# Performance work log

Measured on AMD Instinct MI355X. Metric: run time of the kernel, lower is better.

Reference implementation:

```python
import jax, jax.numpy as jnp
import numpy as np

D_MODEL = 1024   # 'seq_len' arg = input feature dim
FF_DIM = 1024
SCALE = 0.03125  # 1/sqrt(1024)


def setup_inputs() -> dict:
    key = jax.random.key(0)
    ks = jax.random.split(key, 7)
    B, T = 8, 2048
    s = 1.0 / np.sqrt(D_MODEL)
    return {
        "sequence": jax.random.normal(ks[0], (B, T, D_MODEL), dtype=jnp.float32),
        "Wq": jax.random.uniform(ks[1], (FF_DIM, D_MODEL), jnp.float32, -s, s),
        "bq": jax.random.uniform(ks[2], (FF_DIM,), jnp.float32, -s, s),
        "Wk": jax.random.uniform(ks[3], (FF_DIM, D_MODEL), jnp.float32, -s, s),
        "bk": jax.random.uniform(ks[4], (FF_DIM,), jnp.float32, -s, s),
        "Wv": jax.random.uniform(ks[5], (FF_DIM, D_MODEL), jnp.float32, -s, s),
        "bv": jax.random.uniform(ks[6], (FF_DIM,), jnp.float32, -s, s),
    }


def reference(sequence, Wq, bq, Wk, bk, Wv, bv):
    # Q/K/V linear projections (torch Linear: x @ W.T + b)
    q = jnp.einsum('btd,fd->btf', sequence, Wq) + bq
    k = jnp.einsum('btd,fd->btf', sequence, Wk) + bk
    v = jnp.einsum('btd,fd->btf', sequence, Wv) + bv
    # scaled dot-product attention (dropout p=0 -> identity)
    scores = jnp.einsum('btf,bsf->bts', q, k) * SCALE  # [B,T,T]
    attn = jax.nn.softmax(scores, axis=-1)
    return jnp.einsum('bts,bsf->btf', attn, v)
```

## Files before the change

### kernel.cpp

```cpp
#include <hip/hip_runtime.h>
#include <hip/hip_bf16.h>

#define BB 8
#define TT 2048
#define DD 1024
#define FF 1024

typedef __attribute__((ext_vector_type(8))) short bf16x8;
typedef __attribute__((ext_vector_type(4))) float f32x4;
typedef __attribute__((ext_vector_type(4))) short s16x4;

constexpr float kScaleLog2e = 0.03125f * 1.44269504088896340736f;

__device__ __forceinline__ short bf16_bits(float x) {
    __hip_bfloat16 h = __float2bfloat16(x);
    short s;
    __builtin_memcpy(&s, &h, sizeof(short));
    return s;
}

__global__ __launch_bounds__(256) void cvt_all(
    const float* __restrict__ seq, const float* __restrict__ Wq,
    const float* __restrict__ Wk, const float* __restrict__ Wv,
    short* __restrict__ seqb, short* __restrict__ Wb)
{
    const int bid = blockIdx.x;
    const float* src;
    short* dst;
    int i;
    if (bid < 8192)      { src = seq; dst = seqb;                      i = bid * 256 + threadIdx.x; }
    else if (bid < 8704) { src = Wq;  dst = Wb;                        i = (bid - 8192) * 256 + threadIdx.x; }
    else if (bid < 9216) { src = Wk;  dst = Wb + (size_t)FF * DD;      i = (bid - 8704) * 256 + threadIdx.x; }
    else                 { src = Wv;  dst = Wb + (size_t)2 * FF * DD;  i = (bid - 9216) * 256 + threadIdx.x; }
    f32x4 a = ((const f32x4*)src)[2 * i];
    f32x4 b = ((const f32x4*)src)[2 * i + 1];
    bf16x8 o;
#pragma unroll
    for (int j = 0; j < 4; ++j) { o[j] = bf16_bits(a[j]); o[4 + j] = bf16_bits(b[j]); }
    ((bf16x8*)dst)[i] = o;
}

__device__ __forceinline__ void gemm_core(
    const short* __restrict__ A, int lda, int m0,
    const short* __restrict__ B, int ldb, int n0,
    int K, short* As, short* Bs, f32x4 acc[4][4])
{
    const int tid  = threadIdx.x;
    const int lane = tid & 63;
    const int w    = tid >> 6;
    const int wm   = (w & 1) * 64;
    const int wn   = (w >> 1) * 64;
    const int r    = lane & 15;
    const int qd   = lane >> 4;

    for (int k0 = 0; k0 < K; k0 += 64) {
        __syncthreads();
#pragma unroll
        for (int it = 0; it < 4; ++it) {
            const int s   = tid + it * 256;
            const int row = s >> 3;
            const int col = (((s & 7) - (row & 7)) & 7) << 3;
            __builtin_amdgcn_global_load_lds(
                (const __attribute__((address_space(1))) unsigned int*)
                    (A + (size_t)(m0 + row) * lda + k0 + col),
                (__attribute__((address_space(3))) unsigned int*)(As + s * 8),
                16, 0, 0);
            __builtin_amdgcn_global_load_lds(
                (const __attribute__((address_space(1))) unsigned int*)
                    (B + (size_t)(n0 + row) * ldb + k0 + col),
                (__attribute__((address_space(3))) unsigned int*)(Bs + s * 8),
                16, 0, 0);
        }
        __syncthreads();
#pragma unroll
        for (int kk = 0; kk < 2; ++kk) {
            bf16x8 af[4], bf[4];
#pragma unroll
            for (int m = 0; m < 4; ++m) {
                const int R = wm + m * 16 + r;
                af[m] = *(const bf16x8*)(As + R * 64 + (((kk * 4 + qd) + R) & 7) * 8);
            }
#pragma unroll
            for (int n = 0; n < 4; ++n) {
                const int R = wn + n * 16 + r;
                bf[n] = *(const bf16x8*)(Bs + R * 64 + (((kk * 4 + qd) + R) & 7) * 8);
            }
#pragma unroll
            for (int m = 0; m < 4; ++m)
#pragma unroll
                for (int n = 0; n < 4; ++n)
                    acc[m][n] = __builtin_amdgcn_mfma_f32_16x16x32_bf16(af[m], bf[n], acc[m][n], 0, 0, 0);
        }
    }
}

__global__ __launch_bounds__(256) void qkv_tiled(
    const short* __restrict__ seqb, const short* __restrict__ Wb,
    const float* __restrict__ bq, const float* __restrict__ bk,
    const float* __restrict__ bv,
    __hip_bfloat16* __restrict__ q, __hip_bfloat16* __restrict__ k,
    __hip_bfloat16* __restrict__ vT)
{
    __shared__ short As[128 * 64], Bs[128 * 64];
    const int bid  = blockIdx.x;
    const int mt   = bid / 24;
    const int rest = bid % 24;
    const int nt   = rest & 7;
    const int proj = rest >> 3;

    const short* W    = Wb + (size_t)proj * FF * DD;
    const float* bias = proj == 0 ? bq : (proj == 1 ? bk : bv);

    f32x4 acc[4][4];
#pragma unroll
    for (int m = 0; m < 4; ++m)
#pragma unroll
        for (int n = 0; n < 4; ++n) acc[m][n] = (f32x4){0.f, 0.f, 0.f, 0.f};

    gemm_core(seqb, DD, mt * 128, W, DD, nt * 128, DD, As, Bs, acc);

    const int lane = threadIdx.x & 63;
    const int w    = threadIdx.x >> 6;
    const int wm   = (w & 1) * 64;
    const int wn   = (w >> 1) * 64;
    const int r    = lane & 15;
    const int qd   = lane >> 4;
    const int row_base = mt * 128 + wm + qd * 4;
    const int col_base = nt * 128 + wn + r;

    if (proj < 2) {
        __hip_bfloat16* dst = (proj == 0) ? q : k;
#pragma unroll
        for (int n = 0; n < 4; ++n) {
            const int col = col_base + n * 16;
            const float bv_ = bias[col];
#pragma unroll
            for (int m = 0; m < 4; ++m)
#pragma unroll
                for (int i = 0; i < 4; ++i)
                    dst[(size_t)(row_base + m * 16 + i) * FF + col] =
                        __float2bfloat16(acc[m][n][i] + bv_);
        }
    } else {
#pragma unroll
        for (int m = 0; m < 4; ++m) {
            const int rowg = row_base + m * 16;
            const int b_   = rowg >> 11;
            const int t_   = rowg & 2047;
            __hip_bfloat16* vb = vT + (size_t)b_ * FF * TT;
#pragma unroll
            for (int n = 0; n < 4; ++n) {
                const int col = col_base + n * 16;
                const float bv_ = bias[col];
                s16x4 pack;
#pragma unroll
                for (int i = 0; i < 4; ++i) pack[i] = bf16_bits(acc[m][n][i] + bv_);
                *(s16x4*)(vb + (size_t)col * TT + t_) = pack;
            }
        }
    }
}

__global__ __launch_bounds__(256) void score_tiled(
    const __hip_bfloat16* __restrict__ q, const __hip_bfloat16* __restrict__ k,
    __hip_bfloat16* __restrict__ P, float* __restrict__ Z)
{
    __shared__ short As[128 * 64], Bs[128 * 64];
    const int bid = blockIdx.x;
    const int b   = bid >> 8;
    const int rem = bid & 255;
    const int tt  = rem >> 4;
    const int st  = rem & 15;

    const short* qb = (const short*)q + (size_t)b * TT * FF;
    const short* kb = (const short*)k + (size_t)b * TT * FF;

    f32x4 acc[4][4];
#pragma unroll
    for (int m = 0; m < 4; ++m)
#pragma unroll
        for (int n = 0; n < 4; ++n) acc[m][n] = (f32x4){0.f, 0.f, 0.f, 0.f};

    gemm_core(qb, FF, tt * 128, kb, FF, st * 128, FF, As, Bs, acc);

    const int lane = threadIdx.x & 63;
    const int w    = threadIdx.x >> 6;
    const int wm   = (w & 1) * 64;
    const int wn   = (w >> 1) * 64;
    const int r    = lane & 15;
    const int qd   = lane >> 4;
    const int row_base = tt * 128 + wm + qd * 4;
    const int col_base = st * 128 + wn + r;

    __hip_bfloat16* Pb = P + (size_t)b * TT * TT;
    float* Zb = Z + b * TT;

    float rs[4][4];
#pragma unroll
    for (int m = 0; m < 4; ++m)
#pragma unroll
        for (int i = 0; i < 4; ++i) rs[m][i] = 0.f;

#pragma unroll
    for (int m = 0; m < 4; ++m)
#pragma unroll
        for (int n = 0; n < 4; ++n) {
            const int col = col_base + n * 16;
#pragma unroll
            for (int i = 0; i < 4; ++i) {
                const float e = exp2f(acc[m][n][i] * kScaleLog2e);
                const __hip_bfloat16 eb = __float2bfloat16(e);
                rs[m][i] += __bfloat162float(eb);
                Pb[(size_t)(row_base + m * 16 + i) * TT + col] = eb;
            }
        }
#pragma unroll
    for (int off = 1; off < 16; off <<= 1)
#pragma unroll
        for (int m = 0; m < 4; ++m)
#pragma unroll
            for (int i = 0; i < 4; ++i) rs[m][i] += __shfl_xor(rs[m][i], off, 64);
    if (r == 0) {
#pragma unroll
        for (int m = 0; m < 4; ++m)
#pragma unroll
            for (int i = 0; i < 4; ++i)
                atomicAdd(&Zb[row_base + m * 16 + i], rs[m][i]);
    }
}

__global__ __launch_bounds__(256) void pv_tiled(
    const __hip_bfloat16* __restrict__ P, const __hip_bfloat16* __restrict__ vT,
    const float* __restrict__ Z, float* __restrict__ out)
{
    __shared__ short As[128 * 64], Bs[128 * 64];
    const int bid = blockIdx.x;
    const int b   = bid >> 7;
    const int rem = bid & 127;
    const int tt  = rem >> 3;
    const int ft  = rem & 7;

    const short* Pb = (const short*)P + (size_t)b * TT * TT;
    const short* vb = (const short*)vT + (size_t)b * FF * TT;

    f32x4 acc[4][4];
#pragma unroll
    for (int m = 0; m < 4; ++m)
#pragma unroll
        for (int n = 0; n < 4; ++n) acc[m][n] = (f32x4){0.f, 0.f, 0.f, 0.f};

    gemm_core(Pb, TT, tt * 128, vb, TT, ft * 128, TT, As, Bs, acc);

    const int lane = threadIdx.x & 63;
    const int w    = threadIdx.x >> 6;
    const int wm   = (w & 1) * 64;
    const int wn   = (w >> 1) * 64;
    const int r    = lane & 15;
    const int qd   = lane >> 4;
    const int row_base = tt * 128 + wm + qd * 4;
    const int col_base = ft * 128 + wn + r;

    const float* Zb = Z + b * TT;
    float* ob = out + (size_t)b * TT * FF;

#pragma unroll
    for (int m = 0; m < 4; ++m) {
        float rz[4];
#pragma unroll
        for (int i = 0; i < 4; ++i) rz[i] = 1.0f / Zb[row_base + m * 16 + i];
#pragma unroll
        for (int n = 0; n < 4; ++n) {
            const int col = col_base + n * 16;
#pragma unroll
            for (int i = 0; i < 4; ++i)
                ob[(size_t)(row_base + m * 16 + i) * FF + col] = acc[m][n][i] * rz[i];
        }
    }
}

extern "C" void kernel_launch(void* const* d_in, const int* in_sizes, int n_in,
                              void* d_out, int out_size, void* d_ws, size_t ws_size,
                              hipStream_t stream) {
    const float* seq = (const float*)d_in[0];
    const float* Wq  = (const float*)d_in[1];
    const float* bq  = (const float*)d_in[2];
    const float* Wk  = (const float*)d_in[3];
    const float* bk  = (const float*)d_in[4];
    const float* Wv  = (const float*)d_in[5];
    const float* bv  = (const float*)d_in[6];
    float* out = (float*)d_out;
    char* ws = (char*)d_ws;

    const size_t MB32 = 33554432;
    __hip_bfloat16* q   = (__hip_bfloat16*)(ws);
    __hip_bfloat16* k   = (__hip_bfloat16*)(ws + MB32);
    __hip_bfloat16* vT  = (__hip_bfloat16*)(ws + 2 * MB32);
    __hip_bfloat16* P   = (__hip_bfloat16*)(ws + 3 * MB32);
    float*          Z   = (float*)(ws + 3 * MB32 + (size_t)67108864);
    short*          seqb = (short*)P;
    short*          Wb   = (short*)((char*)P + MB32);

    hipMemsetAsync(Z, 0, (size_t)BB * TT * sizeof(float), stream);

    cvt_all<<<9728, 256, 0, stream>>>(seq, Wq, Wk, Wv, seqb, Wb);
    qkv_tiled<<<128 * 24, 256, 0, stream>>>(seqb, Wb, bq, bk, bv, q, k, vT);
    score_tiled<<<BB * 256, 256, 0, stream>>>(q, k, P, Z);
    pv_tiled<<<BB * 128, 256, 0, stream>>>(P, vT, Z, out);
}
```

Baseline: 449.8 us.

## Replace 128x128 GEMM core with 256x256 multi-stage pipelined LDS-DMA GEMM

Replaces the shared GEMM core with a 256x256-tile, 512-thread version. It uses a 4-slot LDS ring of 32-wide K chunks, direct global-to-LDS loads issued three stages ahead, explicit vmcnt waits and raw barriers, setprio around MFMA bursts, and an XOR-swizzled LDS layout. Block IDs are remapped so consecutive blocks spread across XCD groups. The goal is to hide global-load latency behind MFMA work, raise arithmetic intensity per loaded byte, and cut the synchronisation overhead of the old load-sync-compute loop. In exchange, far fewer blocks are launched (256 for PV), which risks tail effects, and the larger register and LDS use per block can lower occupancy.

```diff
diff --git a/kernel.cpp b/kernel.cpp
--- a/kernel.cpp
+++ b/kernel.cpp
@@ -40,240 +40,325 @@
     ((bf16x8*)dst)[i] = o;
 }
 
-__device__ __forceinline__ void gemm_core(
+#define SLOT 8192
+
+__device__ __forceinline__ void stage2(const short* g0, const short* g1,
+                                       short* slot, int lo0, int lo1) {
+    __builtin_amdgcn_global_load_lds(
+        (const __attribute__((address_space(1))) unsigned int*)g0,
+        (__attribute__((address_space(3))) unsigned int*)(slot + lo0), 16, 0, 0);
+    __builtin_amdgcn_global_load_lds(
+        (const __attribute__((address_space(1))) unsigned int*)g1,
+        (__attribute__((address_space(3))) unsigned int*)(slot + lo1), 16, 0, 0);
+}
+
+__device__ __forceinline__ void phase_pre() {
+    __builtin_amdgcn_s_barrier();
+    asm volatile("s_waitcnt lgkmcnt(0)" ::: "memory");
+    __builtin_amdgcn_sched_barrier(0);
+    __builtin_amdgcn_s_setprio(1);
+}
+
+template<int W>
+__device__ __forceinline__ void phase_post() {
+    __builtin_amdgcn_s_setprio(0);
+    __builtin_amdgcn_sched_barrier(0);
+    if constexpr (W == 8)      asm volatile("s_waitcnt vmcnt(8)" ::: "memory");
+    else if constexpr (W == 4) asm volatile("s_waitcnt vmcnt(4)" ::: "memory");
+    else if constexpr (W == 0) asm volatile("s_waitcnt vmcnt(0)" ::: "memory");
+    __builtin_amdgcn_s_barrier();
+}
+
+template<bool S12, bool S34, int W1, int W2>
+__device__ __forceinline__ void tile_body(
+    int t, short* As, short* Bs,
+    const short* a0, const short* a1, const short* b0, const short* b1,
+    int lo0, int lo1, int wm, int wn, int rk, f32x4 (&acc)[8][4])
+{
+    const short* sA0 = As + ((2 * t) & 3) * SLOT;
+    const short* sB0 = Bs + ((2 * t) & 3) * SLOT;
+    const short* sA1 = As + ((2 * t + 1) & 3) * SLOT;
+    const short* sB1 = Bs + ((2 * t + 1) & 3) * SLOT;
+
+    bf16x8 a[4], b[4];
+
+#pragma unroll
+    for (int m = 0; m < 4; ++m) a[m] = *(const bf16x8*)(sA0 + (wm + m * 16) * 32 + rk);
+#pragma unroll
+    for (int n = 0; n < 4; ++n) b[n] = *(const bf16x8*)(sB0 + (wn + n * 16) * 32 + rk);
+    if constexpr (S12)
+        stage2(a0 + (2 * t + 3) * 32, a1 + (2 * t + 3) * 32,
+               As + ((2 * t + 3) & 3) * SLOT, lo0, lo1);
+    phase_pre();
+#pragma unroll
+    for (int m = 0; m < 4; ++m)
+#pragma unroll
+        for (int n = 0; n < 4; ++n)
+            acc[m][n] = __builtin_amdgcn_mfma_f32_16x16x32_bf16(a[m], b[n], acc[m][n], 0, 0, 0);
+    phase_post<-1>();
+
+#pragma unroll
+    for (int m = 0; m < 4; ++m) a[m] = *(const bf16x8*)(sA0 + (wm + 64 + m * 16) * 32 + rk);
+    if constexpr (S12)
+        stage2(b0 + (2 * t + 3) * 32, b1 + (2 * t + 3) * 32,
+               Bs + ((2 * t + 3) & 3) * SLOT, lo0, lo1);
+    phase_pre();
+#pragma unroll
+    for (int m = 0; m < 4; ++m)
+#pragma unroll
+        for (int n = 0; n < 4; ++n)
+            acc[m + 4][n] = __builtin_amdgcn_mfma_f32_16x16x32_bf16(a[m], b[n], acc[m + 4][n], 0, 0, 0);
+    phase_post<W1>();
+
+#pragma unroll
+    for (int m = 0; m < 4; ++m) a[m] = *(const bf16x8*)(sA1 + (wm + m * 16) * 32 + rk);
+#pragma unroll
+    for (int n = 0; n < 4; ++n) b[n] = *(const bf16x8*)(sB1 + (wn + n * 16) * 32 + rk);
+    if constexpr (S34)
+        stage2(a0 + (2 * t + 4) * 32, a1 + (2 * t + 4) * 32,
+               As + ((2 * t + 4) & 3) * SLOT, lo0, lo1);
+    phase_pre();
+#pragma unroll
+    for (int m = 0; m < 4; ++m)
+#pragma unroll
+        for (int n = 0; n < 4; ++n)
+            acc[m][n] = __builtin_amdgcn_mfma_f32_16x16x32_bf16(a[m], b[n], acc[m][n], 0, 0, 0);
+    phase_post<-1>();
+
+#pragma unroll
+    for (int m = 0; m < 4; ++m) a[m] = *(const bf16x8*)(sA1 + (wm + 64 + m * 16) * 32 + rk);
+    if constexpr (S34)
+        stage2(b0 + (2 * t + 4) * 32, b1 + (2 * t + 4) * 32,
+               Bs + ((2 * t + 4) & 3) * SLOT, lo0, lo1);
+    phase_pre();
+#pragma unroll
+    for (int m = 0; m < 4; ++m)
+#pragma unroll
+        for (int n = 0; n < 4; ++n)
+            acc[m + 4][n] = __builtin_amdgcn_mfma_f32_16x16x32_bf16(a[m], b[n], acc[m + 4][n], 0, 0, 0);
+    phase_post<W2>();
+}
+
+__device__ __forceinline__ void gemm256(
     const short* __restrict__ A, int lda, int m0,
     const short* __restrict__ B, int ldb, int n0,
-    int K, short* As, short* Bs, f32x4 acc[4][4])
+    int T, short* As, short* Bs, f32x4 (&acc)[8][4])
 {
     const int tid  = threadIdx.x;
     const int lane = tid & 63;
     const int w    = tid >> 6;
-    const int wm   = (w & 1) * 64;
-    const int wn   = (w >> 1) * 64;
+    const int wm   = (w >> 2) * 128;
+    const int wn   = (w & 3) * 64;
     const int r    = lane & 15;
     const int qd   = lane >> 4;
-
-    for (int k0 = 0; k0 < K; k0 += 64) {
-        __syncthreads();
-#pragma unroll
-        for (int it = 0; it < 4; ++it) {
-            const int s   = tid + it * 256;
-            const int row = s >> 3;
-            const int col = (((s & 7) - (row & 7)) & 7) << 3;
-            __builtin_amdgcn_global_load_lds(
-                (const __attribute__((address_space(1))) unsigned int*)
-                    (A + (size_t)(m0 + row) * lda + k0 + col),
-                (__attribute__((address_space(3))) unsigned int*)(As + s * 8),
-                16, 0, 0);
-            __builtin_amdgcn_global_load_lds(
-                (const __attribute__((address_space(1))) unsigned int*)
-                    (B + (size_t)(n0 + row) * ldb + k0 + col),
-                (__attribute__((address_space(3))) unsigned int*)(Bs + s * 8),
-                16, 0, 0);
-        }
-        __syncthreads();
-#pragma unroll
-        for (int kk = 0; kk < 2; ++kk) {
-            bf16x8 af[4], bf[4];
-#pragma unroll
-            for (int m = 0; m < 4; ++m) {
-                const int R = wm + m * 16 + r;
-                af[m] = *(const bf16x8*)(As + R * 64 + (((kk * 4 + qd) + R) & 7) * 8);
-            }
-#pragma unroll
-            for (int n = 0; n < 4; ++n) {
-                const int R = wn + n * 16 + r;
-                bf[n] = *(const bf16x8*)(Bs + R * 64 + (((kk * 4 + qd) + R) & 7) * 8);
-            }
-#pragma unroll
-            for (int m = 0; m < 4; ++m)
-#pragma unroll
-                for (int n = 0; n < 4; ++n)
-                    acc[m][n] = __builtin_amdgcn_mfma_f32_16x16x32_bf16(af[m], bf[n], acc[m][n], 0, 0, 0);
-        }
-    }
-}
-
-__global__ __launch_bounds__(256) void qkv_tiled(
+    const int rk   = r * 32 + (qd ^ ((r >> 1) & 3)) * 8;
+
+    const int s0   = w * 128 + lane, s1 = s0 + 64;
+    const int row0 = s0 >> 2,  row1 = s1 >> 2;
+    const int cl0  = (s0 & 3) ^ ((row0 >> 1) & 3);
+    const int cl1  = (s1 & 3) ^ ((row1 >> 1) & 3);
+    const short* a0 = A + (size_t)(m0 + row0) * lda + cl0 * 8;
+    const short* a1 = A + (size_t)(m0 + row1) * lda + cl1 * 8;
+    const short* b0 = B + (size_t)(n0 + row0) * ldb + cl0 * 8;
+    const short* b1 = B + (size_t)(n0 + row1) * ldb + cl1 * 8;
+    const int lo0 = s0 * 8, lo1 = s1 * 8;
+
+    stage2(a0,      a1,      As,            lo0, lo1);
+    stage2(b0,      b1,      Bs,            lo0, lo1);
+    stage2(a0 + 32, a1 + 32, As + SLOT,     lo0, lo1);
+    stage2(b0 + 32, b1 + 32, Bs + SLOT,     lo0, lo1);
+    stage2(a0 + 64, a1 + 64, As + 2 * SLOT, lo0, lo1);
+    stage2(b0 + 64, b1 + 64, Bs + 2 * SLOT, lo0, lo1);
+    asm volatile("s_waitcnt vmcnt(8)" ::: "memory");
+    __builtin_amdgcn_s_barrier();
+
+    for (int t = 0; t < T - 2; ++t)
+        tile_body<true, true, 8, 8>(t, As, Bs, a0, a1, b0, b1, lo0, lo1, wm, wn, rk, acc);
+    tile_body<true,  false, 8, 4>(T - 2, As, Bs, a0, a1, b0, b1, lo0, lo1, wm, wn, rk, acc);
+    tile_body<false, false, 0, -1>(T - 1, As, Bs, a0, a1, b0, b1, lo0, lo1, wm, wn, rk, acc);
+}
+
+__global__ __launch_bounds__(512, 2) void qkv256(
     const short* __restrict__ seqb, const short* __restrict__ Wb,
     const float* __restrict__ bq, const float* __restrict__ bk,
     const float* __restrict__ bv,
     __hip_bfloat16* __restrict__ q, __hip_bfloat16* __restrict__ k,
     __hip_bfloat16* __restrict__ vT)
 {
-    __shared__ short As[128 * 64], Bs[128 * 64];
+    __shared__ short As[4 * SLOT], Bs[4 * SLOT];
     const int bid  = blockIdx.x;
-    const int mt   = bid / 24;
-    const int rest = bid % 24;
-    const int nt   = rest & 7;
-    const int proj = rest >> 3;
+    const int id2  = (bid & 7) * 96 + (bid >> 3);
+    const int mt   = id2 / 12;
+    const int rest = id2 - mt * 12;
+    const int nt   = rest & 3;
+    const int proj = rest >> 2;
 
     const short* W    = Wb + (size_t)proj * FF * DD;
     const float* bias = proj == 0 ? bq : (proj == 1 ? bk : bv);
 
-    f32x4 acc[4][4];
-#pragma unroll
-    for (int m = 0; m < 4; ++m)
+    f32x4 acc[8][4];
+#pragma unroll
+    for (int m = 0; m < 8; ++m)
 #pragma unroll
         for (int n = 0; n < 4; ++n) acc[m][n] = (f32x4){0.f, 0.f, 0.f, 0.f};
 
-    gemm_core(seqb, DD, mt * 128, W, DD, nt * 128, DD, As, Bs, acc);
+    gemm256(seqb, DD, mt * 256, W, DD, nt * 256, DD / 64, As, Bs, acc);
 
     const int lane = threadIdx.x & 63;
     const int w    = threadIdx.x >> 6;
-    const int wm   = (w & 1) * 64;
-    const int wn   = (w >> 1) * 64;
+    const int wm   = (w >> 2) * 128;
+    const int wn   = (w & 3) * 64;
     const int r    = lane & 15;
     const int qd   = lane >> 4;
-    const int row_base = mt * 128 + wm + qd * 4;
-    const int col_base = nt * 128 + wn + r;
+    const int row_base = mt * 256 + wm + qd * 4;
+    const int col_base = nt * 256 + wn + r;
 
     if (proj < 2) {
         __hip_bfloat16* dst = (proj == 0) ? q : k;
 #pragma unroll
-        for (int n = 0; n < 4; ++n) {
-            const int col = col_base + n * 16;
+        for (int nf = 0; nf < 4; ++nf) {
+            const int col = col_base + nf * 16;
             const float bv_ = bias[col];
 #pragma unroll
-            for (int m = 0; m < 4; ++m)
+            for (int mf = 0; mf < 8; ++mf)
 #pragma unroll
                 for (int i = 0; i < 4; ++i)
-                    dst[(size_t)(row_base + m * 16 + i) * FF + col] =
-                        __float2bfloat16(acc[m][n][i] + bv_);
+                    dst[(size_t)(row_base + mf * 16 + i) * FF + col] =
+                        __float2bfloat16(acc[mf][nf][i] + bv_);
         }
     } else {
 #pragma unroll
-        for (int m = 0; m < 4; ++m) {
-            const int rowg = row_base + m * 16;
+        for (int mf = 0; mf < 8; ++mf) {
+            const int rowg = row_base + mf * 16;
             const int b_   = rowg >> 11;
             const int t_   = rowg & 2047;
             __hip_bfloat16* vb = vT + (size_t)b_ * FF * TT;
 #pragma unroll
-            for (int n = 0; n < 4; ++n) {
-                const int col = col_base + n * 16;
-                const float bv_ = bias[col];
+            for (int nf = 0; nf < 4; ++nf) {
+                const int col = col_base + nf * 16;
+                const float bvv = bias[col];
                 s16x4 pack;
 #pragma unroll
-                for (int i = 0; i < 4; ++i) pack[i] = bf16_bits(acc[m][n][i] + bv_);
+                for (int i = 0; i < 4; ++i) pack[i] = bf16_bits(acc[mf][nf][i] + bvv);
                 *(s16x4*)(vb + (size_t)col * TT + t_) = pack;
             }
         }
     }
 }
 
-__global__ __launch_bounds__(256) void score_tiled(
+__global__ __launch_bounds__(512, 2) void score256(
     const __hip_bfloat16* __restrict__ q, const __hip_bfloat16* __restrict__ k,
     __hip_bfloat16* __restrict__ P, float* __restrict__ Z)
 {
-    __shared__ short As[128 * 64], Bs[128 * 64];
+    __shared__ short As[4 * SLOT], Bs[4 * SLOT];
     const int bid = blockIdx.x;
-    const int b   = bid >> 8;
-    const int rem = bid & 255;
-    const int tt  = rem >> 4;
-    const int st  = rem & 15;
+    const int id2 = (bid & 7) * 64 + (bid >> 3);
+    const int b   = id2 >> 6;
+    const int tt  = (id2 >> 3) & 7;
+    const int st  = id2 & 7;
 
     const short* qb = (const short*)q + (size_t)b * TT * FF;
     const short* kb = (const short*)k + (size_t)b * TT * FF;
 
-    f32x4 acc[4][4];
-#pragma unroll
-    for (int m = 0; m < 4; ++m)
+    f32x4 acc[8][4];
+#pragma unroll
+    for (int m = 0; m < 8; ++m)
 #pragma unroll
         for (int n = 0; n < 4; ++n) acc[m][n] = (f32x4){0.f, 0.f, 0.f, 0.f};
 
-    gemm_core(qb, FF, tt * 128, kb, FF, st * 128, FF, As, Bs, acc);
+    gemm256(qb, FF, tt * 256, kb, FF, st * 256, FF / 64, As, Bs, acc);
 
     const int lane = threadIdx.x & 63;
     const int w    = threadIdx.x >> 6;
-    const int wm   = (w & 1) * 64;
-    const int wn   = (w >> 1) * 64;
+    const int wm   = (w >> 2) * 128;
+    const int wn   = (w & 3) * 64;
     const int r    = lane & 15;
     const int qd   = lane >> 4;
-    const int row_base = tt * 128 + wm + qd * 4;
-    const int col_base = st * 128 + wn + r;
+    const int row_base = tt * 256 + wm + qd * 4;
+    const int col_base = st * 256 + wn + r;
 
     __hip_bfloat16* Pb = P + (size_t)b * TT * TT;
     float* Zb = Z + b * TT;
 
-    float rs[4][4];
-#pragma unroll
-    for (int m = 0; m < 4; ++m)
-#pragma unroll
-        for (int i = 0; i < 4; ++i) rs[m][i] = 0.f;
-
-#pragma unroll
-    for (int m = 0; m < 4; ++m)
-#pragma unroll
-        for (int n = 0; n < 4; ++n) {
-            const int col = col_base + n * 16;
+    float rs[8][4];
+#pragma unroll
+    for (int mf = 0; mf < 8; ++mf)
+#pragma unroll
+        for (int i = 0; i < 4; ++i) rs[mf][i] = 0.f;
+
+#pragma unroll
+    for (int mf = 0; mf < 8; ++mf)
+#pragma unroll
+        for (int nf = 0; nf < 4; ++nf) {
+            const int col = col_base + nf * 16;
 #pragma unroll
             for (int i = 0; i < 4; ++i) {
-                const float e = exp2f(acc[m][n][i] * kScaleLog2e);
+                const float e = exp2f(acc[mf][nf][i] * kScaleLog2e);
                 const __hip_bfloat16 eb = __float2bfloat16(e);
-                rs[m][i] += __bfloat162float(eb);
-                Pb[(size_t)(row_base + m * 16 + i) * TT + col] = eb;
+                rs[mf][i] += __bfloat162float(eb);
+                Pb[(size_t)(row_base + mf * 16 + i) * TT + col] = eb;
             }
         }
 #pragma unroll
     for (int off = 1; off < 16; off <<= 1)
 #pragma unroll
-        for (int m = 0; m < 4; ++m)
-#pragma unroll
-            for (int i = 0; i < 4; ++i) rs[m][i] += __shfl_xor(rs[m][i], off, 64);
+        for (int mf = 0; mf < 8; ++mf)
+#pragma unroll
+            for (int i = 0; i < 4; ++i) rs[mf][i] += __shfl_xor(rs[mf][i], off, 64);
     if (r == 0) {
 #pragma unroll
-        for (int m = 0; m < 4; ++m)
+        for (int mf = 0; mf < 8; ++mf)
 #pragma unroll
             for (int i = 0; i < 4; ++i)
-                atomicAdd(&Zb[row_base + m * 16 + i], rs[m][i]);
+                atomicAdd(&Zb[row_base + mf * 16 + i], rs[mf][i]);
     }
 }
 
-__global__ __launch_bounds__(256) void pv_tiled(
+__global__ __launch_bounds__(512, 2) void pv256(
     const __hip_bfloat16* __restrict__ P, const __hip_bfloat16* __restrict__ vT,
     const float* __restrict__ Z, float* __restrict__ out)
 {
-    __shared__ short As[128 * 64], Bs[128 * 64];
+    __shared__ short As[4 * SLOT], Bs[4 * SLOT];
     const int bid = blockIdx.x;
-    const int b   = bid >> 7;
-    const int rem = bid & 127;
-    const int tt  = rem >> 3;
-    const int ft  = rem & 7;
+    const int id2 = (bid & 7) * 32 + (bid >> 3);
+    const int b   = id2 >> 5;
+    const int tt  = (id2 >> 2) & 7;
+    const int ft  = id2 & 3;
 
     const short* Pb = (const short*)P + (size_t)b * TT * TT;
     const short* vb = (const short*)vT + (size_t)b * FF * TT;
 
-    f32x4 acc[4][4];
-#pragma unroll
-    for (int m = 0; m < 4; ++m)
+    f32x4 acc[8][4];
+#pragma unroll
+    for (int m = 0; m < 8; ++m)
 #pragma unroll
         for (int n = 0; n < 4; ++n) acc[m][n] = (f32x4){0.f, 0.f, 0.f, 0.f};
 
-    gemm_core(Pb, TT, tt * 128, vb, TT, ft * 128, TT, As, Bs, acc);
+    gemm256(Pb, TT, tt * 256, vb, TT, ft * 256, TT / 64, As, Bs, acc);
 
     const int lane = threadIdx.x & 63;
     const int w    = threadIdx.x >> 6;
-    const int wm   = (w & 1) * 64;
-    const int wn   = (w >> 1) * 64;
+    const int wm   = (w >> 2) * 128;
+    const int wn   = (w & 3) * 64;
     const int r    = lane & 15;
     const int qd   = lane >> 4;
-    const int row_base = tt * 128 + wm + qd * 4;
-    const int col_base = ft * 128 + wn + r;
+    const int row_base = tt * 256 + wm + qd * 4;
+    const int col_base = ft * 256 + wn + r;
 
     const float* Zb = Z + b * TT;
     float* ob = out + (size_t)b * TT * FF;
 
 #pragma unroll
-    for (int m = 0; m < 4; ++m) {
+    for (int mf = 0; mf < 8; ++mf) {
         float rz[4];
 #pragma unroll
-        for (int i = 0; i < 4; ++i) rz[i] = 1.0f / Zb[row_base + m * 16 + i];
-#pragma unroll
-        for (int n = 0; n < 4; ++n) {
-            const int col = col_base + n * 16;
+        for (int i = 0; i < 4; ++i) rz[i] = 1.0f / Zb[row_base + mf * 16 + i];
+#pragma unroll
+        for (int nf = 0; nf < 4; ++nf) {
+            const int col = col_base + nf * 16;
 #pragma unroll
             for (int i = 0; i < 4; ++i)
-                ob[(size_t)(row_base + m * 16 + i) * FF + col] = acc[m][n][i] * rz[i];
+                ob[(size_t)(row_base + mf * 16 + i) * FF + col] = acc[mf][nf][i] * rz[i];
         }
     }
 }
@@ -303,7 +388,7 @@
     hipMemsetAsync(Z, 0, (size_t)BB * TT * sizeof(float), stream);
 
     cvt_all<<<9728, 256, 0, stream>>>(seq, Wq, Wk, Wv, seqb, Wb);
-    qkv_tiled<<<128 * 24, 256, 0, stream>>>(seqb, Wb, bq, bk, bv, q, k, vT);
-    score_tiled<<<BB * 256, 256, 0, stream>>>(q, k, P, Z);
-    pv_tiled<<<BB * 128, 256, 0, stream>>>(P, vT, Z, out);
-}
+    qkv256<<<768, 512, 0, stream>>>(seqb, Wb, bq, bk, bv, q, k, vT);
+    score256<<<BB * 64, 512, 0, stream>>>(q, k, P, Z);
+    pv256<<<BB * 32, 512, 0, stream>>>(P, vT, Z, out);
+}
```

New measurement: 429.1 us. 4.6% less time.
